# Kernel optimization log

Measured on AMD Instinct MI355X. Metric: run time of the kernel, lower is better.

## Reference

```python
import jax, jax.numpy as jnp
import numpy as np
import math

H = 32       # num_attention_heads
HKV = 8      # num_key_value_heads
D = 128      # attention_head_size


def setup_inputs() -> dict:
    key = jax.random.key(0)
    k1, k2, k3 = jax.random.split(key, 3)
    B, L = 2, 2048
    return {
        "query_states": jax.random.normal(k1, (B, L, H * D), dtype=jnp.float32),
        "key_states": jax.random.normal(k2, (B, L, HKV * D), dtype=jnp.float32),
        "value_states": jax.random.normal(k3, (B, L, HKV * D), dtype=jnp.float32),
    }


def reference(query_states, key_states, value_states):
    B, L, _ = query_states.shape
    groups = H // HKV

    # view + transpose(1,2): (B, heads, L, D)
    q = query_states.reshape(B, L, H, D).transpose(0, 2, 1, 3)
    k = key_states.reshape(B, L, HKV, D).transpose(0, 2, 1, 3)
    v = value_states.reshape(B, L, HKV, D).transpose(0, 2, 1, 3)

    # repeat_kv: repeat_interleave along head dim
    k = jnp.repeat(k, groups, axis=1)
    v = jnp.repeat(v, groups, axis=1)

    q = q.astype(jnp.float16)
    k = k.astype(jnp.float16)
    v = v.astype(jnp.float16)

    # source: transpose(1,2) -> (B, L, H, D), then reshape(B*H, L, D)
    # (row-major reshape of the (B,L,H,D) layout, replicated exactly)
    q = q.transpose(0, 2, 1, 3).reshape(B * H, L, D)
    k = k.transpose(0, 2, 1, 3).reshape(B * H, L, D)
    v = v.transpose(0, 2, 1, 3).reshape(B * H, L, D)

    scale = 1.0 / math.sqrt(D)
    attn_scores = jnp.einsum("bqd,bkd->bqk", q, k) * jnp.float16(scale)
    attn_weights = jax.nn.softmax(attn_scores, axis=-1)
    attn_output = jnp.einsum("bqk,bkd->bqd", attn_weights, v)

    # reshape(B,H,L,D).transpose(1,2) -> (B,L,H,D) -> (B, L, H*D)
    attn_output = attn_output.reshape(B, H, L, D).transpose(0, 2, 1, 3)
    return attn_output.reshape(B, L, H * D)
```

## Files before the change

kernel.cpp:

```cpp
#include <hip/hip_runtime.h>
#include <hip/hip_bf16.h>

typedef _Float16 f16;
typedef f16 f16x2 __attribute__((ext_vector_type(2)));
typedef f16 f16x4 __attribute__((ext_vector_type(4)));
typedef f16 f16x8 __attribute__((ext_vector_type(8)));
typedef float f32x4 __attribute__((ext_vector_type(4)));

#define NB   2
#define LL   2048
#define LQ   2048
#define LKV  512
#define DD   128
#define BM   128
#define BN   64
#define KS_STR 132
#define VT_STR 68
#define PT_STR 68

__global__ __launch_bounds__(256, 2)
void fa_fwd(const float* __restrict__ qg,
            const float* __restrict__ kg,
            const float* __restrict__ vg,
            float* __restrict__ og)
{
    __shared__ __align__(16) f16 smem[BN*KS_STR + DD*VT_STR + BM*PT_STR];
    f16* Ks = smem;
    f16* Vt = smem + BN*KS_STR;
    f16* Pt = smem + BN*KS_STR + DD*VT_STR;

    const int tid  = threadIdx.x;
    const int wave = tid >> 6;
    const int lane = tid & 63;
    const int ln   = lane & 15;
    const int qd   = lane >> 4;

    const int qt   = blockIdx.x;
    const int g    = blockIdx.y;
    const int bb   = g >> 5;
    const int lhi  = g & 31;

    const float* qmat = qg + (size_t)(bb*LL + 64*lhi)*4096;
    const float* kmat = kg + (size_t)(bb*LL + 64*lhi)*1024;
    const float* vmat = vg + (size_t)(bb*LL + 64*lhi)*1024;

    const int qbase = qt*BM + wave*32;

    f16x8 qf[2][4];
#pragma unroll
    for (int nt = 0; nt < 2; ++nt) {
        const float* qrow = qmat + (size_t)(qbase + 16*nt + ln)*DD;
#pragma unroll
        for (int kc = 0; kc < 4; ++kc) {
            const float4* qp = (const float4*)(qrow + kc*32 + 8*qd);
            float4 f0 = qp[0], f1 = qp[1];
            f16x8 t = { (f16)f0.x,(f16)f0.y,(f16)f0.z,(f16)f0.w,
                        (f16)f1.x,(f16)f1.y,(f16)f1.z,(f16)f1.w };
            qf[nt][kc] = t;
        }
    }

    f32x4 o[2][8];
#pragma unroll
    for (int nt = 0; nt < 2; ++nt)
#pragma unroll
        for (int dmt = 0; dmt < 8; ++dmt)
#pragma unroll
            for (int r = 0; r < 4; ++r) o[nt][dmt][r] = 0.0f;

    float mrun[2] = {-1e30f, -1e30f}, lrun[2] = {0.0f, 0.0f};
    const float SC2 = 0.08837890625f * 1.44269504088896340f;

    for (int kt = 0; kt < LKV/BN; ++kt) {
        const float* kb = kmat + kt*BN*DD;
        const float* vb = vmat + kt*BN*DD;

#pragma unroll
        for (int i = 0; i < 8; ++i) {
            int f = tid + i*256;
            int row = f >> 5, c4 = f & 31;
            float4 x = *(const float4*)(kb + f*4);
            f16x4 h4 = { (f16)x.x,(f16)x.y,(f16)x.z,(f16)x.w };
            *(f16x4*)(Ks + row*KS_STR + c4*4) = h4;
        }
#pragma unroll
        for (int i = 0; i < 8; ++i) {
            int f = tid + i*256;
            int kvr = f & 63, c4 = f >> 6;
            float4 x = *(const float4*)(vb + (size_t)kvr*DD + c4*4);
            Vt[(c4*4+0)*VT_STR + kvr] = (f16)x.x;
            Vt[(c4*4+1)*VT_STR + kvr] = (f16)x.y;
            Vt[(c4*4+2)*VT_STR + kvr] = (f16)x.z;
            Vt[(c4*4+3)*VT_STR + kvr] = (f16)x.w;
        }
        __syncthreads();

        f32x4 st[2][4];
#pragma unroll
        for (int nt = 0; nt < 2; ++nt)
#pragma unroll
            for (int mt = 0; mt < 4; ++mt)
#pragma unroll
                for (int r = 0; r < 4; ++r) st[nt][mt][r] = 0.0f;
#pragma unroll
        for (int mt = 0; mt < 4; ++mt) {
            const f16* kr = Ks + (16*mt + ln)*KS_STR + 8*qd;
#pragma unroll
            for (int kc = 0; kc < 4; ++kc) {
                f16x4 a0 = *(const f16x4*)(kr + kc*32);
                f16x4 a1 = *(const f16x4*)(kr + kc*32 + 4);
                f16x8 af = __builtin_shufflevector(a0, a1, 0,1,2,3,4,5,6,7);
#pragma unroll
                for (int nt = 0; nt < 2; ++nt)
                    st[nt][mt] = __builtin_amdgcn_mfma_f32_16x16x32_f16(af, qf[nt][kc], st[nt][mt], 0,0,0);
            }
        }

        float alph[2];
#pragma unroll
        for (int nt = 0; nt < 2; ++nt) {
            float mx = -1e30f;
#pragma unroll
            for (int mt = 0; mt < 4; ++mt)
#pragma unroll
                for (int r = 0; r < 4; ++r) {
                    float v = st[nt][mt][r]*SC2; st[nt][mt][r] = v; mx = fmaxf(mx, v);
                }
            mx = fmaxf(mx, __shfl_xor(mx, 16, 64));
            mx = fmaxf(mx, __shfl_xor(mx, 32, 64));
            float mnew = fmaxf(mrun[nt], mx);
            alph[nt] = exp2f(mrun[nt] - mnew);
            float rs = 0.0f;
#pragma unroll
            for (int mt = 0; mt < 4; ++mt)
#pragma unroll
                for (int r = 0; r < 4; ++r) {
                    float p = exp2f(st[nt][mt][r] - mnew);
                    st[nt][mt][r] = p; rs += p;
                }
            rs += __shfl_xor(rs, 16, 64);
            rs += __shfl_xor(rs, 32, 64);
            lrun[nt] = lrun[nt]*alph[nt] + rs;
            mrun[nt] = mnew;
        }

#pragma unroll
        for (int nt = 0; nt < 2; ++nt) {
            f16* prow = Pt + (wave*32 + 16*nt + ln)*PT_STR + 4*qd;
#pragma unroll
            for (int mt = 0; mt < 4; ++mt)
#pragma unroll
                for (int p2 = 0; p2 < 2; ++p2) {
                    f16x2 pp = { (f16)st[nt][mt][2*p2], (f16)st[nt][mt][2*p2+1] };
                    *(f16x2*)(prow + 16*mt + 2*p2) = pp;
                }
        }

#pragma unroll
        for (int nt = 0; nt < 2; ++nt)
#pragma unroll
            for (int dmt = 0; dmt < 8; ++dmt)
#pragma unroll
                for (int r = 0; r < 4; ++r) o[nt][dmt][r] *= alph[nt];

#pragma unroll
        for (int kc2 = 0; kc2 < 2; ++kc2) {
            f16x8 pf[2];
#pragma unroll
            for (int nt = 0; nt < 2; ++nt) {
                const f16* pr = Pt + (wave*32 + 16*nt + ln)*PT_STR + kc2*32 + 8*qd;
                f16x4 b0 = *(const f16x4*)(pr);
                f16x4 b1 = *(const f16x4*)(pr + 4);
                pf[nt] = __builtin_shufflevector(b0, b1, 0,1,2,3,4,5,6,7);
            }
#pragma unroll
            for (int dmt = 0; dmt < 8; ++dmt) {
                const f16* vr = Vt + (16*dmt + ln)*VT_STR + kc2*32 + 8*qd;
                f16x4 a0 = *(const f16x4*)(vr);
                f16x4 a1 = *(const f16x4*)(vr + 4);
                f16x8 vf = __builtin_shufflevector(a0, a1, 0,1,2,3,4,5,6,7);
#pragma unroll
                for (int nt = 0; nt < 2; ++nt)
                    o[nt][dmt] = __builtin_amdgcn_mfma_f32_16x16x32_f16(vf, pf[nt], o[nt][dmt], 0,0,0);
            }
        }
        __syncthreads();
    }

#pragma unroll
    for (int nt = 0; nt < 2; ++nt) {
        float inv = 1.0f / lrun[nt];
        int qtok = qbase + 16*nt + ln;
        float* orow = og + (size_t)(bb*LL + qtok)*4096 + lhi*DD + 4*qd;
#pragma unroll
        for (int dmt = 0; dmt < 8; ++dmt) {
            float4 x = { o[nt][dmt][0]*inv, o[nt][dmt][1]*inv,
                         o[nt][dmt][2]*inv, o[nt][dmt][3]*inv };
            *(float4*)(orow + 16*dmt) = x;
        }
    }
}

extern "C" void kernel_launch(void* const* d_in, const int* in_sizes, int n_in,
                              void* d_out, int out_size, void* d_ws, size_t ws_size,
                              hipStream_t stream) {
    (void)in_sizes; (void)n_in; (void)out_size; (void)d_ws; (void)ws_size;
    const float* q = (const float*)d_in[0];
    const float* k = (const float*)d_in[1];
    const float* v = (const float*)d_in[2];
    float* o = (float*)d_out;
    dim3 grid(LQ/BM, 64, 1), block(256);
    hipLaunchKernelGGL(fa_fwd, grid, block, 0, stream, q, k, v, o);
}
```

Baseline: 213.7 us.

## Pre-convert K and transposed V to fp16 workspace and swizzle LDS tiles

Adds a prep kernel that converts K to fp16 and V to a transposed fp16 layout once per head group, writing both to workspace. Before this, each of the 16 query-tile blocks per group repeated that conversion. The attention kernel now loads fp16 tiles with 16-byte vector loads into XOR-swizzled unpadded LDS, which shrinks shared memory and allows 3 blocks per CU. It also widens the P stores and reads. The cost is an extra kernel launch, workspace traffic, and reliance on a large enough d_ws.

```diff
diff --git a/kernel.cpp b/kernel.cpp
--- a/kernel.cpp
+++ b/kernel.cpp
@@ -2,32 +2,68 @@
 #include <hip/hip_bf16.h>
 
 typedef _Float16 f16;
-typedef f16 f16x2 __attribute__((ext_vector_type(2)));
 typedef f16 f16x4 __attribute__((ext_vector_type(4)));
 typedef f16 f16x8 __attribute__((ext_vector_type(8)));
 typedef float f32x4 __attribute__((ext_vector_type(4)));
 
-#define NB   2
 #define LL   2048
 #define LQ   2048
 #define LKV  512
 #define DD   128
 #define BM   128
 #define BN   64
-#define KS_STR 132
-#define VT_STR 68
-#define PT_STR 68
-
-__global__ __launch_bounds__(256, 2)
+#define PT_STR 72
+
+
+__global__ __launch_bounds__(256)
+void prep(const float* __restrict__ kg, const float* __restrict__ vg,
+          f16* __restrict__ kws, f16* __restrict__ vtws)
+{
+    const int kt = blockIdx.x;
+    const int g  = blockIdx.y;
+    const int bb = g >> 5, lhi = g & 31;
+    const int tid = threadIdx.x;
+    const float* kb = kg + ((size_t)bb*LL + 64*lhi)*1024 + (size_t)kt*BN*DD;
+    const float* vb = vg + ((size_t)bb*LL + 64*lhi)*1024 + (size_t)kt*BN*DD;
+    f16* kd = kws  + ((size_t)g*8 + kt)*8192;
+    f16* vd = vtws + ((size_t)g*8 + kt)*8192;
+
+#pragma unroll
+    for (int i = 0; i < 8; ++i) {
+        int f = tid + i*256;
+        float4 x = *(const float4*)(kb + f*4);
+        f16x4 h = { (f16)x.x,(f16)x.y,(f16)x.z,(f16)x.w };
+        *(f16x4*)(kd + f*4) = h;
+    }
+    __shared__ f16 vt[8192];
+#pragma unroll
+    for (int i = 0; i < 8; ++i) {
+        int f = tid + i*256;
+        int kvr = f & 63, c4 = f >> 6;
+        float4 x = *(const float4*)(vb + (size_t)kvr*DD + c4*4);
+        vt[(c4*4+0)*64 + kvr] = (f16)x.x;
+        vt[(c4*4+1)*64 + kvr] = (f16)x.y;
+        vt[(c4*4+2)*64 + kvr] = (f16)x.z;
+        vt[(c4*4+3)*64 + kvr] = (f16)x.w;
+    }
+    __syncthreads();
+#pragma unroll
+    for (int i = 0; i < 4; ++i) {
+        int f = tid + i*256;
+        *(f16x8*)(vd + f*8) = *(const f16x8*)(vt + f*8);
+    }
+}
+
+__global__ __launch_bounds__(256, 3)
 void fa_fwd(const float* __restrict__ qg,
-            const float* __restrict__ kg,
-            const float* __restrict__ vg,
+            const f16* __restrict__ kws,
+            const f16* __restrict__ vtws,
             float* __restrict__ og)
 {
-    __shared__ __align__(16) f16 smem[BN*KS_STR + DD*VT_STR + BM*PT_STR];
+    __shared__ __align__(16) f16 smem[8192 + 8192 + BM*PT_STR];
     f16* Ks = smem;
-    f16* Vt = smem + BN*KS_STR;
-    f16* Pt = smem + BN*KS_STR + DD*VT_STR;
+    f16* Vt = smem + 8192;
+    f16* Pt = smem + 16384;
 
     const int tid  = threadIdx.x;
     const int wave = tid >> 6;
@@ -40,9 +76,9 @@
     const int bb   = g >> 5;
     const int lhi  = g & 31;
 
-    const float* qmat = qg + (size_t)(bb*LL + 64*lhi)*4096;
-    const float* kmat = kg + (size_t)(bb*LL + 64*lhi)*1024;
-    const float* vmat = vg + (size_t)(bb*LL + 64*lhi)*1024;
+    const float* qmat = qg + ((size_t)bb*LL + 64*lhi)*4096;
+    const f16* ktiles = kws  + (size_t)g*8*8192;
+    const f16* vtiles = vtws + (size_t)g*8*8192;
 
     const int qbase = qt*BM + wave*32;
 
@@ -72,26 +108,22 @@
     const float SC2 = 0.08837890625f * 1.44269504088896340f;
 
     for (int kt = 0; kt < LKV/BN; ++kt) {
-        const float* kb = kmat + kt*BN*DD;
-        const float* vb = vmat + kt*BN*DD;
-
-#pragma unroll
-        for (int i = 0; i < 8; ++i) {
+        const f16* ktile = ktiles + kt*8192;
+        const f16* vtile = vtiles + kt*8192;
+
+#pragma unroll
+        for (int i = 0; i < 4; ++i) {
             int f = tid + i*256;
-            int row = f >> 5, c4 = f & 31;
-            float4 x = *(const float4*)(kb + f*4);
-            f16x4 h4 = { (f16)x.x,(f16)x.y,(f16)x.z,(f16)x.w };
-            *(f16x4*)(Ks + row*KS_STR + c4*4) = h4;
-        }
-#pragma unroll
-        for (int i = 0; i < 8; ++i) {
+            int row = f >> 4, cb = f & 15;
+            f16x8 h = *(const f16x8*)(ktile + f*8);
+            *(f16x8*)(Ks + row*128 + ((cb ^ (row & 15)) * 8)) = h;
+        }
+#pragma unroll
+        for (int i = 0; i < 4; ++i) {
             int f = tid + i*256;
-            int kvr = f & 63, c4 = f >> 6;
-            float4 x = *(const float4*)(vb + (size_t)kvr*DD + c4*4);
-            Vt[(c4*4+0)*VT_STR + kvr] = (f16)x.x;
-            Vt[(c4*4+1)*VT_STR + kvr] = (f16)x.y;
-            Vt[(c4*4+2)*VT_STR + kvr] = (f16)x.z;
-            Vt[(c4*4+3)*VT_STR + kvr] = (f16)x.w;
+            int row = f >> 3, vb = f & 7;
+            f16x8 h = *(const f16x8*)(vtile + f*8);
+            *(f16x8*)(Vt + row*64 + ((vb ^ (row & 7)) * 8)) = h;
         }
         __syncthreads();
 
@@ -104,12 +136,10 @@
                 for (int r = 0; r < 4; ++r) st[nt][mt][r] = 0.0f;
 #pragma unroll
         for (int mt = 0; mt < 4; ++mt) {
-            const f16* kr = Ks + (16*mt + ln)*KS_STR + 8*qd;
+            const f16* kr = Ks + (16*mt + ln)*128;
 #pragma unroll
             for (int kc = 0; kc < 4; ++kc) {
-                f16x4 a0 = *(const f16x4*)(kr + kc*32);
-                f16x4 a1 = *(const f16x4*)(kr + kc*32 + 4);
-                f16x8 af = __builtin_shufflevector(a0, a1, 0,1,2,3,4,5,6,7);
+                f16x8 af = *(const f16x8*)(kr + (((4*kc + qd) ^ ln) * 8));
 #pragma unroll
                 for (int nt = 0; nt < 2; ++nt)
                     st[nt][mt] = __builtin_amdgcn_mfma_f32_16x16x32_f16(af, qf[nt][kc], st[nt][mt], 0,0,0);
@@ -148,12 +178,11 @@
         for (int nt = 0; nt < 2; ++nt) {
             f16* prow = Pt + (wave*32 + 16*nt + ln)*PT_STR + 4*qd;
 #pragma unroll
-            for (int mt = 0; mt < 4; ++mt)
-#pragma unroll
-                for (int p2 = 0; p2 < 2; ++p2) {
-                    f16x2 pp = { (f16)st[nt][mt][2*p2], (f16)st[nt][mt][2*p2+1] };
-                    *(f16x2*)(prow + 16*mt + 2*p2) = pp;
-                }
+            for (int mt = 0; mt < 4; ++mt) {
+                f16x4 pp = { (f16)st[nt][mt][0], (f16)st[nt][mt][1],
+                             (f16)st[nt][mt][2], (f16)st[nt][mt][3] };
+                *(f16x4*)(prow + 16*mt) = pp;
+            }
         }
 
 #pragma unroll
@@ -167,18 +196,12 @@
         for (int kc2 = 0; kc2 < 2; ++kc2) {
             f16x8 pf[2];
 #pragma unroll
-            for (int nt = 0; nt < 2; ++nt) {
-                const f16* pr = Pt + (wave*32 + 16*nt + ln)*PT_STR + kc2*32 + 8*qd;
-                f16x4 b0 = *(const f16x4*)(pr);
-                f16x4 b1 = *(const f16x4*)(pr + 4);
-                pf[nt] = __builtin_shufflevector(b0, b1, 0,1,2,3,4,5,6,7);
-            }
+            for (int nt = 0; nt < 2; ++nt)
+                pf[nt] = *(const f16x8*)(Pt + (wave*32 + 16*nt + ln)*PT_STR + kc2*32 + 8*qd);
 #pragma unroll
             for (int dmt = 0; dmt < 8; ++dmt) {
-                const f16* vr = Vt + (16*dmt + ln)*VT_STR + kc2*32 + 8*qd;
-                f16x4 a0 = *(const f16x4*)(vr);
-                f16x4 a1 = *(const f16x4*)(vr + 4);
-                f16x8 vf = __builtin_shufflevector(a0, a1, 0,1,2,3,4,5,6,7);
+                const f16* vr = Vt + (16*dmt + ln)*64;
+                f16x8 vf = *(const f16x8*)(vr + (((4*kc2 + qd) ^ (ln & 7)) * 8));
 #pragma unroll
                 for (int nt = 0; nt < 2; ++nt)
                     o[nt][dmt] = __builtin_amdgcn_mfma_f32_16x16x32_f16(vf, pf[nt], o[nt][dmt], 0,0,0);
@@ -191,7 +214,7 @@
     for (int nt = 0; nt < 2; ++nt) {
         float inv = 1.0f / lrun[nt];
         int qtok = qbase + 16*nt + ln;
-        float* orow = og + (size_t)(bb*LL + qtok)*4096 + lhi*DD + 4*qd;
+        float* orow = og + ((size_t)bb*LL + qtok)*4096 + lhi*DD + 4*qd;
 #pragma unroll
         for (int dmt = 0; dmt < 8; ++dmt) {
             float4 x = { o[nt][dmt][0]*inv, o[nt][dmt][1]*inv,
@@ -204,11 +227,15 @@
 extern "C" void kernel_launch(void* const* d_in, const int* in_sizes, int n_in,
                               void* d_out, int out_size, void* d_ws, size_t ws_size,
                               hipStream_t stream) {
-    (void)in_sizes; (void)n_in; (void)out_size; (void)d_ws; (void)ws_size;
+    (void)in_sizes; (void)n_in; (void)out_size; (void)ws_size;
     const float* q = (const float*)d_in[0];
     const float* k = (const float*)d_in[1];
     const float* v = (const float*)d_in[2];
     float* o = (float*)d_out;
-    dim3 grid(LQ/BM, 64, 1), block(256);
-    hipLaunchKernelGGL(fa_fwd, grid, block, 0, stream, q, k, v, o);
+    f16* kws  = (f16*)d_ws;
+    f16* vtws = (f16*)d_ws + (size_t)64*8*8192;
+    dim3 pgrid(8, 64), pblk(256);
+    hipLaunchKernelGGL(prep, pgrid, pblk, 0, stream, k, v, kws, vtws);
+    dim3 grid(LQ/BM, 64), block(256);
+    hipLaunchKernelGGL(fa_fwd, grid, block, 0, stream, q, kws, vtws, o);
 }
```

Result: slower. 226.8 us (+6.2%).
